# Optimization experiments

Measured on AMD Instinct MI355X. Metric: run time of the kernel, lower is better.

Reference implementation:

```python
import jax, jax.numpy as jnp
import numpy as np


def conv1x1(x, w, b):
    # x: [B,Cin,H,W], w: [Cout,Cin], b: [Cout]
    return jnp.einsum('bchw,oc->bohw', x, w) + b[None, :, None, None]


def _lin_idx_w(in_size, out_size):
    # PyTorch bilinear, align_corners=False: src = max((i+0.5)*scale - 0.5, 0)
    scale = in_size / out_size
    src = jnp.maximum((jnp.arange(out_size, dtype=jnp.float32) + 0.5) * scale - 0.5, 0.0)
    i0 = jnp.floor(src).astype(jnp.int32)
    i0 = jnp.minimum(i0, in_size - 1)
    i1 = jnp.minimum(i0 + 1, in_size - 1)
    w1 = src - i0.astype(jnp.float32)
    return i0, i1, w1


def bilinear_resize(x, out_h, out_w):
    Hin, Win = x.shape[-2], x.shape[-1]
    y0, y1, wy = _lin_idx_w(Hin, out_h)
    x0, x1, wx = _lin_idx_w(Win, out_w)
    wy = wy[:, None]  # [out_h,1]
    rows = x[:, :, y0, :] * (1.0 - wy) + x[:, :, y1, :] * wy
    out = rows[:, :, :, x0] * (1.0 - wx) + rows[:, :, :, x1] * wx      # [B,C,out_h,out_w]
    return out


def setup_inputs() -> dict:
    key = jax.random.key(0)
    ks = jax.random.split(key, 10)
    C, C8 = 512, 64
    s = 1.0 / np.sqrt(C)
    return {
        'content': jax.random.normal(ks[0], (4, C, 64, 64), jnp.float32),
        'style': jax.random.normal(ks[1], (4, C, 80, 80), jnp.float32),
        'f_w': jax.random.normal(ks[2], (C8, C), jnp.float32) * s,
        'f_b': jax.random.normal(ks[3], (C8,), jnp.float32) * 0.01,
        'g_w': jax.random.normal(ks[4], (C8, C), jnp.float32) * s,
        'g_b': jax.random.normal(ks[5], (C8,), jnp.float32) * 0.01,
        'h_w': jax.random.normal(ks[6], (C, C), jnp.float32) * s,
        'h_b': jax.random.normal(ks[7], (C,), jnp.float32) * 0.01,
        'out_w': jax.random.normal(ks[8], (C, C), jnp.float32) * s,
        'out_b': jax.random.normal(ks[9], (C,), jnp.float32) * 0.01,
    }


def reference(content, style, f_w, f_b, g_w, g_b, h_w, h_b, out_w, out_b):
    B, C, H, W = content.shape
    HW = H * W
    f = conv1x1(content, f_w, f_b).reshape(B, -1, HW)                       # [B,C8,HW] (query, pre-transpose)
    g = bilinear_resize(conv1x1(style, g_w, g_b), H, W).reshape(B, -1, HW)  # [B,C8,HW]
    h = bilinear_resize(conv1x1(style, h_w, h_b), H, W).reshape(B, C, HW)   # [B,C,HW]
    attn = jax.nn.softmax(jnp.einsum('bcm,bcn->bmn', f, g), axis=-1)        # [B,HW_q,HW_k]
    out = jnp.einsum('bcn,bmn->bcm', h, attn).reshape(B, C, H, W)
    return conv1x1(out, out_w, out_b)
```

## Files before the change

### kernel.cpp

```cpp
#include <hip/hip_runtime.h>

#define NB 4
#define NC 512
#define ND 64
#define HW 4096
#define SPIN 6400

typedef _Float16 f16;
typedef _Float16 f16x8 __attribute__((ext_vector_type(8)));
typedef short s16x8 __attribute__((ext_vector_type(8)));
typedef short s16x4 __attribute__((ext_vector_type(4)));
typedef float f32x4 __attribute__((ext_vector_type(4)));
typedef float f32x16 __attribute__((ext_vector_type(16)));
typedef unsigned short ushortT;

__device__ __forceinline__ unsigned short f32_to_bf16(float x) {
  union { float f; unsigned u; } v; v.f = x;
  unsigned r = v.u + 0x7FFFu + ((v.u >> 16) & 1u);
  return (unsigned short)(r >> 16);
}

__device__ __forceinline__ void stv(float* p, float v) { *p = v; }
__device__ __forceinline__ void stv(f16* p, float v) { *p = (f16)v; }
__device__ __forceinline__ void stv(unsigned short* p, float v) { *p = f32_to_bf16(v); }

__device__ __forceinline__ unsigned cvt_pk_bf16(float lo, float hi) {
  unsigned r;
  asm("v_cvt_pk_bf16_f32 %0, %1, %2" : "=v"(r) : "v"(lo), "v"(hi));
  return r;
}

#if __has_builtin(__builtin_amdgcn_exp2f)
#define EXP2F(x) __builtin_amdgcn_exp2f(x)
#else
#define EXP2F(x) exp2f(x)
#endif

__global__ __launch_bounds__(256) void cvtw_kernel(const float* __restrict__ fw,
                                                   const float* __restrict__ gw,
                                                   const float* __restrict__ hw,
                                                   const float* __restrict__ ow,
                                                   f16* __restrict__ dst) {
  int i = blockIdx.x * 256 + threadIdx.x;
  const float* src; int off;
  if (i < 32768) { src = fw; off = 0; }
  else if (i < 65536) { src = gw; off = 32768; }
  else if (i < 327680) { src = hw; off = 65536; }
  else { src = ow; off = 327680; }
  dst[i] = (f16)src[i - off];
}

__global__ __launch_bounds__(256) void tcvt_kernel(const float* __restrict__ in,
                                                   f16* __restrict__ out) {
  __shared__ float Xs[64][65];
  int p0 = blockIdx.x * 64, c0 = blockIdx.y * 64, b = blockIdx.z;
  int t = threadIdx.x;
  const float* ib = in + ((size_t)b * NC + c0) * HW + p0;
  int pl = t & 63, cg = t >> 6;
#pragma unroll
  for (int k = 0; k < 16; ++k) {
    int c = cg * 16 + k;
    Xs[c][pl] = ib[(size_t)c * HW + pl];
  }
  __syncthreads();
  int p = t >> 2, cb = (t & 3) * 16;
  union { f16 h[16]; float4 q[2]; } u;
#pragma unroll
  for (int j = 0; j < 16; ++j) u.h[j] = (f16)Xs[cb + j][p];
  f16* ob = out + ((size_t)b * HW + p0 + p) * NC + c0 + cb;
  *(float4*)(ob) = u.q[0];
  *(float4*)(ob + 8) = u.q[1];
}

__global__ __launch_bounds__(256) void rstcvt_kernel(const float* __restrict__ X,
                                                     f16* __restrict__ Y) {
  __shared__ float Xs[64 * 165];
  int oy = blockIdx.x, c0 = blockIdx.y * 64, b = blockIdx.z;
  float syf = fmaxf((oy + 0.5f) * 1.25f - 0.5f, 0.f);
  int y0 = (int)syf; int y1 = min(y0 + 1, 79); float wy = syf - (float)y0;
  int t = threadIdx.x;
  const float* Xb = X + ((size_t)b * NC + c0) * SPIN;
#pragma unroll
  for (int k = 0; k < 10; ++k) {
    int idx = t + k * 256;
    int c = idx / 40;
    int rem = idx - c * 40;
    int yy = rem / 20;
    int x4 = rem - yy * 20;
    int ysrc = yy ? y1 : y0;
    float4 v = *(const float4*)(Xb + (size_t)c * SPIN + ysrc * 80 + x4 * 4);
    float* d = Xs + c * 165 + yy * 82 + x4 * 4;
    d[0] = v.x; d[1] = v.y; d[2] = v.z; d[3] = v.w;
  }
  __syncthreads();
  int ox = t >> 2, cb = (t & 3) * 16;
  float sxf = fmaxf((ox + 0.5f) * 1.25f - 0.5f, 0.f);
  int x0 = (int)sxf; int x1 = min(x0 + 1, 79); float wx = sxf - (float)x0;
  union { f16 h[16]; float4 q[2]; } u;
#pragma unroll
  for (int j = 0; j < 16; ++j) {
    const float* base = Xs + (cb + j) * 165;
    float a0 = base[x0], a1 = base[x1];
    float b0 = base[82 + x0], b1 = base[82 + x1];
    float r0 = a0 + (a1 - a0) * wx;
    float r1 = b0 + (b1 - b0) * wx;
    u.h[j] = (f16)(r0 + (r1 - r0) * wy);
  }
  f16* ob = Y + ((size_t)b * HW + oy * 64 + ox) * NC + c0 + cb;
  *(float4*)(ob) = u.q[0];
  *(float4*)(ob + 8) = u.q[1];
}

__global__ __launch_bounds__(256) void convpm2_kernel(const f16* __restrict__ X0,
                                                      const f16* __restrict__ X1,
                                                      const f16* __restrict__ W01,
                                                      const float* __restrict__ b0,
                                                      const float* __restrict__ b1,
                                                      f16* __restrict__ Y0,
                                                      f16* __restrict__ Y1) {
  int sel = blockIdx.z >> 2;
  int b = blockIdx.z & 3;
  const f16* X = sel ? X1 : X0;
  const f16* W = W01 + sel * (ND * NC);
  const float* bias = sel ? b1 : b0;
  f16* Y = sel ? Y1 : Y0;
  int t = threadIdx.x, l = t & 63, w = t >> 6;
  int pw = blockIdx.x * 256 + w * 64;
  int l4 = l & 15, g = l >> 4;
  f32x4 acc[4][4] = {};
  const f16* Xb = X + ((size_t)b * HW + pw) * NC;
  for (int kk = 0; kk < 16; ++kk) {
    int co = kk * 32 + g * 8;
    f16x8 a[4], bb[4];
#pragma unroll
    for (int ms = 0; ms < 4; ++ms) a[ms] = *(const f16x8*)(Xb + (size_t)(ms * 16 + l4) * NC + co);
#pragma unroll
    for (int ct = 0; ct < 4; ++ct) bb[ct] = *(const f16x8*)(W + (size_t)(ct * 16 + l4) * NC + co);
#pragma unroll
    for (int ms = 0; ms < 4; ++ms)
#pragma unroll
      for (int ct = 0; ct < 4; ++ct)
        acc[ms][ct] = __builtin_amdgcn_mfma_f32_16x16x32_f16(a[ms], bb[ct], acc[ms][ct], 0, 0, 0);
  }
  float bv[4];
#pragma unroll
  for (int ct = 0; ct < 4; ++ct) bv[ct] = bias[ct * 16 + l4];
  f16* Yb = Y + ((size_t)b * HW + pw) * ND;
#pragma unroll
  for (int ms = 0; ms < 4; ++ms)
#pragma unroll
    for (int ct = 0; ct < 4; ++ct)
#pragma unroll
      for (int r = 0; r < 4; ++r)
        Yb[(size_t)(ms * 16 + g * 4 + r) * ND + ct * 16 + l4] = (f16)(acc[ms][ct][r] + bv[ct]);
}

template <typename OUT_T>
__global__ __launch_bounds__(256) void convcm_kernel(const f16* __restrict__ X,
                                                     const f16* __restrict__ W,
                                                     const float* __restrict__ bias,
                                                     OUT_T* __restrict__ Y, int O) {
  int b = blockIdx.z;
  int o0 = blockIdx.x * 64;
  int t = threadIdx.x, l = t & 63, w = t >> 6;
  int pw = blockIdx.y * 256 + w * 64;
  int l4 = l & 15, g = l >> 4;
  f32x4 acc[4][4] = {};
  const f16* Xb = X + ((size_t)b * HW + pw) * NC;
  const f16* Wb = W + (size_t)o0 * NC;
  for (int kk = 0; kk < 16; ++kk) {
    int co = kk * 32 + g * 8;
    f16x8 a[4], bb[4];
#pragma unroll
    for (int ms = 0; ms < 4; ++ms) a[ms] = *(const f16x8*)(Wb + (size_t)(ms * 16 + l4) * NC + co);
#pragma unroll
    for (int ct = 0; ct < 4; ++ct) bb[ct] = *(const f16x8*)(Xb + (size_t)(ct * 16 + l4) * NC + co);
#pragma unroll
    for (int ms = 0; ms < 4; ++ms)
#pragma unroll
      for (int ct = 0; ct < 4; ++ct)
        acc[ms][ct] = __builtin_amdgcn_mfma_f32_16x16x32_f16(a[ms], bb[ct], acc[ms][ct], 0, 0, 0);
  }
  float bv[4][4];
#pragma unroll
  for (int ms = 0; ms < 4; ++ms)
#pragma unroll
    for (int r = 0; r < 4; ++r) bv[ms][r] = bias[o0 + ms * 16 + g * 4 + r];
#pragma unroll
  for (int ms = 0; ms < 4; ++ms)
#pragma unroll
    for (int ct = 0; ct < 4; ++ct)
#pragma unroll
      for (int r = 0; r < 4; ++r) {
        float val = acc[ms][ct][r] + bv[ms][r];
        stv(&Y[((size_t)b * O + o0 + ms * 16 + g * 4 + r) * HW + pw + ct * 16 + l4], val);
      }
}

union PAu { unsigned u[4]; s16x8 v; };
union VSu { s16x8 v; s16x4 h[2]; };

__global__ __launch_bounds__(256, 2) void attn_kernel(const f16* __restrict__ FT,
                                                      const f16* __restrict__ GT,
                                                      const unsigned short* __restrict__ HC,
                                                      f16* __restrict__ MIDT) {
  __shared__ __align__(16) char Vs[2][32768];
  int bid = blockIdx.x;
  int b = (bid & 7) >> 1;
  int cs = bid & 1;
  int mt = bid >> 3;
  int t = threadIdx.x, l = t & 63, w = t >> 6;
  int lm = l & 31, hf = l >> 5;
  int mf = w >> 1, cq = w & 1;
  int mr = mt * 64 + mf * 32;
  int cqb = cq * 128;

  const f16* Fq = FT + ((size_t)b * HW + mr + lm) * ND + hf * 8;
  f16x8 q[4];
  {
    const f16 l2e = (f16)1.44269504f;
#pragma unroll
    for (int kc = 0; kc < 4; ++kc) {
      f16x8 v = *(const f16x8*)(Fq + kc * 16);
#pragma unroll
      for (int j = 0; j < 8; ++j) v[j] *= l2e;
      q[kc] = v;
    }
  }

  const f16* kp0 = GT + (size_t)b * HW * ND + (size_t)lm * ND + hf * 8;
  const f16* kp1 = kp0 + 32 * ND;

  int scv = t >> 2;
  int nsg = (t & 3) * 16;
  const unsigned short* vp0 = HC + ((size_t)b * NC + cs * 256 + scv) * HW + nsg;
  const unsigned short* vp1 = vp0 + (size_t)64 * HW;
  const unsigned short* vp2 = vp0 + (size_t)128 * HW;
  const unsigned short* vp3 = vp0 + (size_t)192 * HW;

  int sb0 = (t & 3) * 32;
  int swv = (scv & 7) << 4;
  char* wa = Vs[0] + scv * 128 + (sb0 ^ swv);
  char* wb = Vs[0] + scv * 128 + ((sb0 + 16) ^ swv);

  int cl0 = cqb + lm;
  int vsw = (lm & 7) << 4;
  const char* r0 = Vs[0] + cl0 * 128 + ((0 + hf * 16) ^ vsw);
  const char* r1 = Vs[0] + cl0 * 128 + ((32 + hf * 16) ^ vsw);
  const char* r2 = Vs[0] + cl0 * 128 + ((64 + hf * 16) ^ vsw);
  const char* r3 = Vs[0] + cl0 * 128 + ((96 + hf * 16) ^ vsw);

  f32x16 acc[4] = {};
  float den = 0.f;

#define KLOAD(KN)                                                          \
  do {                                                                     \
    _Pragma("unroll") for (int kc = 0; kc < 4; ++kc) {                     \
      KN[0][kc] = *(const f16x8*)(kp0 + kc * 16);                          \
      KN[1][kc] = *(const f16x8*)(kp1 + kc * 16);                          \
    }                                                                      \
    kp0 += 64 * ND; kp1 += 64 * ND;                                        \
  } while (0)

#define VLOAD()                                                            \
  do {                                                                     \
    vreg[0].v = *(const s16x8*)(vp0); vreg[1].v = *(const s16x8*)(vp0 + 8);\
    vreg[2].v = *(const s16x8*)(vp1); vreg[3].v = *(const s16x8*)(vp1 + 8);\
    vreg[4].v = *(const s16x8*)(vp2); vreg[5].v = *(const s16x8*)(vp2 + 8);\
    vreg[6].v = *(const s16x8*)(vp3); vreg[7].v = *(const s16x8*)(vp3 + 8);\
    vp0 += 64; vp1 += 64; vp2 += 64; vp3 += 64;                            \
  } while (0)

#define VWRITE(BOFF)                                                       \
  do {                                                                     \
    _Pragma("unroll") for (int r_ = 0; r_ < 4; ++r_) {                     \
      *(s16x4*)(wa + (BOFF) + r_ * 8192) = vreg[2 * r_].h[0];              \
      *(s16x4*)(wb + (BOFF) + r_ * 8192) = vreg[2 * r_].h[1];              \
      *(s16x4*)(wa + (BOFF) + r_ * 8192 + 8) = vreg[2 * r_ + 1].h[0];      \
      *(s16x4*)(wb + (BOFF) + r_ * 8192 + 8) = vreg[2 * r_ + 1].h[1];      \
    }                                                                      \
  } while (0)

#define PACK(sv, PA, o)                                                    \
  do {                                                                     \
    float p_[16];                                                          \
    _Pragma("unroll") for (int r_ = 0; r_ < 16; ++r_) p_[r_] = EXP2F(sv[r_]); \
    float d0_ = (p_[0] + p_[1]) + (p_[2] + p_[3]);                         \
    float d1_ = (p_[4] + p_[5]) + (p_[6] + p_[7]);                         \
    float d2_ = (p_[8] + p_[9]) + (p_[10] + p_[11]);                       \
    float d3_ = (p_[12] + p_[13]) + (p_[14] + p_[15]);                     \
    den += (d0_ + d1_) + (d2_ + d3_);                                      \
    PA[o].u[0] = cvt_pk_bf16(p_[0], p_[1]);                                \
    PA[o].u[1] = cvt_pk_bf16(p_[2], p_[3]);                                \
    PA[o].u[2] = cvt_pk_bf16(p_[4], p_[5]);                                \
    PA[o].u[3] = cvt_pk_bf16(p_[6], p_[7]);                                \
    PA[o + 1].u[0] = cvt_pk_bf16(p_[8], p_[9]);                            \
    PA[o + 1].u[1] = cvt_pk_bf16(p_[10], p_[11]);                          \
    PA[o + 1].u[2] = cvt_pk_bf16(p_[12], p_[13]);                          \
    PA[o + 1].u[3] = cvt_pk_bf16(p_[14], p_[15]);                          \
  } while (0)

#define PVBODY(PA, BOFF)                                                   \
  do {                                                                     \
    _Pragma("unroll") for (int cf = 0; cf < 4; ++cf) {                     \
      s16x8 v0_ = *(const s16x8*)(r0 + (BOFF) + cf * 4096);                \
      s16x8 v1_ = *(const s16x8*)(r1 + (BOFF) + cf * 4096);                \
      s16x8 v2_ = *(const s16x8*)(r2 + (BOFF) + cf * 4096);                \
      s16x8 v3_ = *(const s16x8*)(r3 + (BOFF) + cf * 4096);                \
      __builtin_amdgcn_s_setprio(1);                                       \
      acc[cf] = __builtin_amdgcn_mfma_f32_32x32x16_bf16(PA[0].v, v0_, acc[cf], 0, 0, 0); \
      acc[cf] = __builtin_amdgcn_mfma_f32_32x32x16_bf16(PA[1].v, v1_, acc[cf], 0, 0, 0); \
      acc[cf] = __builtin_amdgcn_mfma_f32_32x32x16_bf16(PA[2].v, v2_, acc[cf], 0, 0, 0); \
      acc[cf] = __builtin_amdgcn_mfma_f32_32x32x16_bf16(PA[3].v, v3_, acc[cf], 0, 0, 0); \
      __builtin_amdgcn_s_setprio(0);                                       \
    }                                                                      \
  } while (0)

#define ITER(PC, PP, KC, KN, BOFF, PRE, DOPV)                              \
  do {                                                                     \
    VSu vreg[8];                                                           \
    if (PRE) { KLOAD(KN); VLOAD(); }                                       \
    f32x16 s0 = {}, s1 = {};                                               \
    __builtin_amdgcn_s_setprio(1);                                         \
    _Pragma("unroll") for (int kc = 0; kc < 4; ++kc)                       \
        s0 = __builtin_amdgcn_mfma_f32_32x32x16_f16(KC[0][kc], q[kc], s0, 0, 0, 0); \
    _Pragma("unroll") for (int kc = 0; kc < 4; ++kc)                       \
        s1 = __builtin_amdgcn_mfma_f32_32x32x16_f16(KC[1][kc], q[kc], s1, 0, 0, 0); \
    __builtin_amdgcn_s_setprio(0);                                         \
    if (DOPV) PVBODY(PP, BOFF);                                            \
    PACK(s0, PC, 0);                                                       \
    PACK(s1, PC, 2);                                                       \
    __syncthreads();                                                       \
    if (PRE) VWRITE(BOFF);                                                 \
  } while (0)

  {
    VSu vreg[8];
    VLOAD();
    VWRITE(0);
  }
  f16x8 kbA[2][4], kbB[2][4];
  KLOAD(kbA);
  __syncthreads();

  PAu paA[4], paB[4];
  ITER(paA, paB, kbA, kbB, 32768, true, false);
  for (int ito = 0; ito < 31; ++ito) {
    ITER(paB, paA, kbB, kbA, 0, true, true);
    ITER(paA, paB, kbA, kbB, 32768, true, true);
  }
  ITER(paB, paA, kbB, kbA, 0, false, true);
  PVBODY(paB, 32768);

#undef KLOAD
#undef VLOAD
#undef VWRITE
#undef PACK
#undef PVBODY
#undef ITER

  den += __shfl_xor(den, 32);
  float rd = 1.f / den;
  f16* Mb = MIDT + ((size_t)b * HW + mr) * NC + cs * 256 + cqb + lm;
#pragma unroll
  for (int r = 0; r < 16; ++r) {
    int mrow = (r & 3) + 8 * (r >> 2) + 4 * hf;
    float rv = __shfl(rd, mrow);
#pragma unroll
    for (int cf = 0; cf < 4; ++cf)
      Mb[(size_t)mrow * NC + cf * 32] = (f16)(acc[cf][r] * rv);
  }
}

extern "C" void kernel_launch(void* const* d_in, const int* in_sizes, int n_in,
                              void* d_out, int out_size, void* d_ws, size_t ws_size,
                              hipStream_t stream) {
  const float* content = (const float*)d_in[0];
  const float* style   = (const float*)d_in[1];
  const float* f_w = (const float*)d_in[2];
  const float* f_b = (const float*)d_in[3];
  const float* g_w = (const float*)d_in[4];
  const float* g_b = (const float*)d_in[5];
  const float* h_w = (const float*)d_in[6];
  const float* h_b = (const float*)d_in[7];
  const float* out_w = (const float*)d_in[8];
  const float* out_b = (const float*)d_in[9];
  float* out = (float*)d_out;

  const size_t MB = 1ull << 20;
  char* base = (char*)d_ws;
  f16* contentT = (f16*)base;
  f16* midT     = (f16*)base;
  unsigned short* hC = (unsigned short*)(base + 16 * MB);
  f16* fT = (f16*)(base + 32 * MB);
  f16* gT = (f16*)(base + 34 * MB);
  f16* styrT = (f16*)(base + 48 * MB);
  f16* w16 = (f16*)(base + 64 * MB);
  f16* fw16 = w16;
  f16* gw16 = w16 + 32768;
  f16* hw16 = w16 + 65536;
  f16* ow16 = w16 + 327680;

  cvtw_kernel<<<dim3(589824 / 256), 256, 0, stream>>>(f_w, g_w, h_w, out_w, w16);
  tcvt_kernel<<<dim3(HW / 64, NC / 64, NB), 256, 0, stream>>>(content, contentT);
  rstcvt_kernel<<<dim3(64, NC / 64, NB), 256, 0, stream>>>(style, styrT);
  convpm2_kernel<<<dim3(HW / 256, 1, 2 * NB), 256, 0, stream>>>(contentT, styrT, fw16, f_b, g_b, fT, gT);
  convcm_kernel<unsigned short><<<dim3(NC / 64, HW / 256, NB), 256, 0, stream>>>(styrT, hw16, h_b, hC, NC);
  attn_kernel<<<dim3(512), 256, 0, stream>>>(fT, gT, hC, midT);
  convcm_kernel<float><<<dim3(NC / 64, HW / 256, NB), 256, 0, stream>>>(midT, ow16, out_b, out, NC);
}
```

Before: 285.5 us.

## Use barrier without vmcnt drain and remap V tile loads

```diff
diff --git a/kernel.cpp b/kernel.cpp
--- a/kernel.cpp
+++ b/kernel.cpp
@@ -35,6 +35,9 @@
 #else
 #define EXP2F(x) exp2f(x)
 #endif
+
+#define BARRIER_NODRAIN() \
+  asm volatile("s_waitcnt lgkmcnt(0)\n\ts_barrier" ::: "memory")
 
 __global__ __launch_bounds__(256) void cvtw_kernel(const float* __restrict__ fw,
                                                    const float* __restrict__ gw,
@@ -231,17 +234,13 @@
   const f16* kp0 = GT + (size_t)b * HW * ND + (size_t)lm * ND + hf * 8;
   const f16* kp1 = kp0 + 32 * ND;
 
-  int scv = t >> 2;
-  int nsg = (t & 3) * 16;
-  const unsigned short* vp0 = HC + ((size_t)b * NC + cs * 256 + scv) * HW + nsg;
-  const unsigned short* vp1 = vp0 + (size_t)64 * HW;
-  const unsigned short* vp2 = vp0 + (size_t)128 * HW;
-  const unsigned short* vp3 = vp0 + (size_t)192 * HW;
-
-  int sb0 = (t & 3) * 32;
-  int swv = (scv & 7) << 4;
-  char* wa = Vs[0] + scv * 128 + (sb0 ^ swv);
-  char* wb = Vs[0] + scv * 128 + ((sb0 + 16) ^ swv);
+  int sc = t >> 3;
+  int nseg = (t & 7) * 8;
+  int sb0 = ((nseg >> 4) * 32) + (((nseg >> 3) & 1) * 8);
+  int swv = (sc & 7) << 4;
+  const unsigned short* vp = HC + ((size_t)b * NC + cs * 256 + sc) * HW + nseg;
+  char* wa = Vs[0] + sc * 128 + (sb0 ^ swv);
+  char* wbp = Vs[0] + sc * 128 + ((sb0 + 16) ^ swv);
 
   int cl0 = cqb + lm;
   int vsw = (lm & 7) << 4;
@@ -264,20 +263,16 @@
 
 #define VLOAD()                                                            \
   do {                                                                     \
-    vreg[0].v = *(const s16x8*)(vp0); vreg[1].v = *(const s16x8*)(vp0 + 8);\
-    vreg[2].v = *(const s16x8*)(vp1); vreg[3].v = *(const s16x8*)(vp1 + 8);\
-    vreg[4].v = *(const s16x8*)(vp2); vreg[5].v = *(const s16x8*)(vp2 + 8);\
-    vreg[6].v = *(const s16x8*)(vp3); vreg[7].v = *(const s16x8*)(vp3 + 8);\
-    vp0 += 64; vp1 += 64; vp2 += 64; vp3 += 64;                            \
+    _Pragma("unroll") for (int r_ = 0; r_ < 8; ++r_)                       \
+        vreg[r_].v = *(const s16x8*)(vp + (size_t)r_ * 32 * HW);           \
+    vp += 64;                                                              \
   } while (0)
 
 #define VWRITE(BOFF)                                                       \
   do {                                                                     \
-    _Pragma("unroll") for (int r_ = 0; r_ < 4; ++r_) {                     \
-      *(s16x4*)(wa + (BOFF) + r_ * 8192) = vreg[2 * r_].h[0];              \
-      *(s16x4*)(wb + (BOFF) + r_ * 8192) = vreg[2 * r_].h[1];              \
-      *(s16x4*)(wa + (BOFF) + r_ * 8192 + 8) = vreg[2 * r_ + 1].h[0];      \
-      *(s16x4*)(wb + (BOFF) + r_ * 8192 + 8) = vreg[2 * r_ + 1].h[1];      \
+    _Pragma("unroll") for (int r_ = 0; r_ < 8; ++r_) {                     \
+      *(s16x4*)(wa + (BOFF) + r_ * 4096) = vreg[r_].h[0];                  \
+      *(s16x4*)(wbp + (BOFF) + r_ * 4096) = vreg[r_].h[1];                 \
     }                                                                      \
   } while (0)
 
@@ -330,7 +325,7 @@
     if (DOPV) PVBODY(PP, BOFF);                                            \
     PACK(s0, PC, 0);                                                       \
     PACK(s1, PC, 2);                                                       \
-    __syncthreads();                                                       \
+    BARRIER_NODRAIN();                                                     \
     if (PRE) VWRITE(BOFF);                                                 \
   } while (0)
 
@@ -341,7 +336,7 @@
   }
   f16x8 kbA[2][4], kbB[2][4];
   KLOAD(kbA);
-  __syncthreads();
+  BARRIER_NODRAIN();
 
   PAu paA[4], paB[4];
   ITER(paA, paB, kbA, kbB, 32768, true, false);
```

Result: slower. 326.5 us (+14.3%).
